# Performance work log

Measured on AMD Instinct MI355X. Metric: run time of the kernel, lower is better.

## Reference

```python
import jax, jax.numpy as jnp
import numpy as np

PS = 7  # patch (window) size
NH = 8  # num heads for local attention
EPS = 1e-5


def _rel_index(ps):
    # standard Swin-style relative position index over a ps x ps window
    coords = np.stack(np.meshgrid(np.arange(ps), np.arange(ps), indexing='ij'))  # (2,ps,ps)
    flat = coords.reshape(2, -1)                                # (2, ps*ps)
    rel = (flat[:, :, None] - flat[:, None, :]).transpose(1, 2, 0)  # (N,N,2)
    rel[..., 0] += ps - 1
    rel[..., 1] += ps - 1
    rel[..., 0] *= 2 * ps - 1
    return rel.sum(-1)  # (N,N) values in [0,(2ps-1)^2)

REL_IDX = jnp.asarray(_rel_index(PS))  # (49,49)


def _mha(x, qkv_w, qkv_b, proj_w, proj_b, num_heads, bias):
    # x: (Bn, N, C); weights stored (in,out)
    Bn, N, C = x.shape
    d = C // num_heads
    qkv = (x @ qkv_w + qkv_b).reshape(Bn, N, 3, num_heads, d).transpose(2, 0, 3, 1, 4)
    q, k, v = qkv[0], qkv[1], qkv[2]
    attn = jnp.einsum('bhnd,bhmd->bhnm', q, k) * (d ** -0.5)
    if bias is not None:
        attn = attn + bias
    attn = jax.nn.softmax(attn, axis=-1)
    out = jnp.einsum('bhnm,bhmd->bhnd', attn, v).transpose(0, 2, 1, 3).reshape(Bn, N, C)
    return out @ proj_w + proj_b


def setup_inputs() -> dict:
    key = jax.random.key(0)
    ks = jax.random.split(key, 8)
    B, C, H, W = 4, 256, 112, 112
    s = 0.02
    return {
        'x': jax.random.normal(ks[0], (B, C, H, W), jnp.float32),
        'norm_gamma': jnp.ones((C,), jnp.float32),
        'norm_beta': jnp.zeros((C,), jnp.float32),
        'qkv_l_w': jax.random.normal(ks[1], (C, 3 * C), jnp.float32) * s,
        'qkv_l_b': jnp.zeros((3 * C,), jnp.float32),
        'proj_l_w': jax.random.normal(ks[2], (C, C), jnp.float32) * s,
        'proj_l_b': jnp.zeros((C,), jnp.float32),
        'rpb_table': jax.random.normal(ks[3], ((2 * PS - 1) ** 2, NH), jnp.float32) * s,
        'qkv_c_w': jax.random.normal(ks[4], (PS * PS, 3 * PS * PS), jnp.float32) * s,
        'qkv_c_b': jnp.zeros((3 * PS * PS,), jnp.float32),
        'proj_c_w': jax.random.normal(ks[5], (PS * PS, PS * PS), jnp.float32) * s,
        'proj_c_b': jnp.zeros((PS * PS,), jnp.float32),
        'proj_w': jax.random.normal(ks[6], (2 * C, C), jnp.float32) * s,
    }


def reference(x, norm_gamma, norm_beta, qkv_l_w, qkv_l_b, proj_l_w, proj_l_b,
              rpb_table, qkv_c_w, qkv_c_b, proj_c_w, proj_c_b, proj_w):
    B, C, H, W = x.shape
    ps, N = PS, PS * PS
    nP = (H // ps) * (W // ps)
    shortcut = x

    # b c h w -> b h w c, then LayerNorm over C
    xt = x.transpose(0, 2, 3, 1)
    mu = xt.mean(-1, keepdims=True)
    var = xt.var(-1, keepdims=True)
    xn = (xt - mu) * jax.lax.rsqrt(var + EPS) * norm_gamma + norm_beta

    # window partition -> (B*nP, N, C)
    patches = xn.reshape(B, H // ps, ps, W // ps, ps, C)
    patches = patches.transpose(0, 1, 3, 2, 4, 5).reshape(-1, N, C)

    # local windowed attention with relative position bias
    bias = rpb_table[REL_IDX].transpose(2, 0, 1)[None]  # (1,NH,N,N)
    attn_local = _mha(patches, qkv_l_w, qkv_l_b, proj_l_w, proj_l_b, NH, bias)

    # cross-channel attention: (B*C, nP, N), dim=N, single head, no RPE
    pc = patches.reshape(B, nP, N, C).transpose(0, 3, 1, 2).reshape(B * C, nP, N)
    attn_cross = _mha(pc, qkv_c_w, qkv_c_b, proj_c_w, proj_c_b, 1, None)
    attn_cross = attn_cross.reshape(B, C, nP, N).transpose(0, 2, 3, 1).reshape(-1, N, C)

    def reverse(w):  # (B*nP, N, C) -> (B, H*W, C)
        w = w.reshape(B, H // ps, W // ps, ps, ps, C)
        return w.transpose(0, 1, 3, 2, 4, 5).reshape(B, H * W, C)

    out = jnp.concatenate([reverse(attn_local), reverse(attn_cross)], axis=-1) @ proj_w
    out = out.reshape(B, H, W, C).transpose(0, 3, 1, 2)
    return (out, shortcut)
```

## Files before the change

### kernel.cpp

```cpp
#include <hip/hip_runtime.h>
#include <hip/hip_bf16.h>


#define PS 7
#define NWIN_N 49
#define CH 256
#define HH 112
#define WW 112
#define BB 4
#define NHEAD 8
#define HD 32

static constexpr size_t ELEMS = (size_t)BB * CH * HH * WW;
static constexpr size_t SZ    = ELEMS * 2;

typedef __attribute__((ext_vector_type(8))) short short8;
typedef __attribute__((ext_vector_type(4))) float f32x4;

static __device__ __forceinline__ unsigned short bf16_bits(float v) {
    __hip_bfloat16 h = __float2bfloat16(v);
    return *reinterpret_cast<unsigned short*>(&h);
}

__global__ __launch_bounds__(256) void ln_partition_kernel(
    const float* __restrict__ x, const float* __restrict__ gamma,
    const float* __restrict__ beta, __hip_bfloat16* __restrict__ patches)
{
    int blk = blockIdx.x;
    int seg = blk % 7;
    int bh = blk / 7;
    int h = bh % HH, b = bh / HH;
    int w0 = seg * 16;
    int tid = threadIdx.x;

    __shared__ float X[256][17];
    __shared__ float mus[16], rstds[16];

    #pragma unroll
    for (int l = 0; l < 16; ++l) {
        int idx = l * 256 + tid;
        int c = idx >> 4, wl = idx & 15;
        X[c][wl] = x[((size_t)(b * CH + c) * HH + h) * WW + w0 + wl];
    }
    __syncthreads();

    if (tid < 16) {
        float s = 0.f, ss = 0.f;
        for (int c = 0; c < 256; ++c) { float v = X[c][tid]; s += v; ss += v * v; }
        float mu = s * (1.f / 256.f);
        float var = ss * (1.f / 256.f) - mu * mu;
        mus[tid] = mu;
        rstds[tid] = rsqrtf(var + 1e-5f);
    }
    __syncthreads();

    int c = tid;
    float g = gamma[c], be = beta[c];
    int hp = h / PS, r = h - hp * PS;
    #pragma unroll
    for (int wl = 0; wl < 16; ++wl) {
        int w = w0 + wl;
        int wp = w / PS, cc = w - wp * PS;
        int win = (b * 16 + hp) * 16 + wp;
        int i = r * PS + cc;
        float v = (X[c][wl] - mus[wl]) * rstds[wl] * g + be;
        patches[((size_t)win * NWIN_N + i) * CH + c] = __float2bfloat16(v);
    }
}

__global__ __launch_bounds__(256) void copy_f32_kernel(
    const float* __restrict__ x, float* __restrict__ out)
{
    size_t i = ((size_t)blockIdx.x * 256 + threadIdx.x) * 4;
    *(float4*)(out + i) = *(const float4*)(x + i);
}

__global__ __launch_bounds__(256) void prep_wt_kernel(
    const float* __restrict__ W, unsigned short* __restrict__ Wt,
    int Kreal, int N, int Kpad, int Npad)
{
    int idx = blockIdx.x * 256 + threadIdx.x;
    if (idx >= Npad * Kpad) return;
    int n = idx / Kpad, k = idx - n * Kpad;
    float v = (n < N && k < Kreal) ? W[(size_t)k * N + n] : 0.f;
    Wt[idx] = bf16_bits(v);
}

__global__ __launch_bounds__(256) void prep_wt_qkvc_kernel(
    const float* __restrict__ W, unsigned short* __restrict__ Wt)
{
    int idx = blockIdx.x * 256 + threadIdx.x;
    if (idx >= 192 * 64) return;
    int n = idx >> 6, k = idx & 63;
    int s = -1;
    if (n < 49) s = n;
    else if (n >= 56 && n < 105) s = n - 7;
    else if (n >= 112 && n < 161) s = n - 14;
    float v = (s >= 0 && k < 49) ? W[(size_t)k * 147 + s] : 0.f;
    Wt[idx] = bf16_bits(v);
}

__global__ __launch_bounds__(192) void prep_bias_c_kernel(
    const float* __restrict__ b, float* __restrict__ bc)
{
    int n = threadIdx.x;
    int s = -1;
    if (n < 49) s = n;
    else if (n >= 56 && n < 105) s = n - 7;
    else if (n >= 112 && n < 161) s = n - 14;
    bc[n] = (s >= 0) ? b[s] : 0.f;
}

__global__ __launch_bounds__(256) void bias_prep_kernel(
    const float* __restrict__ rpb, float* __restrict__ biasb)
{
    int idx = blockIdx.x * 256 + threadIdx.x;
    int head = idx >> 12;
    int rem = idx & 4095;
    int i = rem >> 6, j = rem & 63;
    float v;
    if (j >= NWIN_N) v = -1e9f;
    else if (i >= NWIN_N) v = 0.f;
    else {
        int ri = i / 7, ci = i - ri * 7;
        int rj = j / 7, cj = j - rj * 7;
        v = rpb[((ri - rj + 6) * 13 + (ci - cj + 6)) * NHEAD + head];
    }
    biasb[idx] = v;
}

__global__ __launch_bounds__(256) void pad49_kernel(
    const unsigned short* __restrict__ src, unsigned short* __restrict__ dst)
{
    size_t idx = (size_t)blockIdx.x * 256 + threadIdx.x;
    int t = idx & 63;
    size_t m = idx >> 6;
    dst[idx] = (t < 49) ? src[m * 49 + t] : (unsigned short)0;
}

__global__ __launch_bounds__(256) void gemm_mfma_kernel(
    const __hip_bfloat16* __restrict__ A1p, const __hip_bfloat16* __restrict__ A2p,
    int K1, const unsigned short* __restrict__ Wt, const float* __restrict__ bias,
    __hip_bfloat16* __restrict__ Cb, float* __restrict__ Cf,
    int M, int N, int K, int pitchN)
{
    __shared__ __align__(16) unsigned short Alds[128][72];
    __shared__ __align__(16) unsigned short Wlds[64][72];
    const unsigned short* A1 = (const unsigned short*)A1p;
    const unsigned short* A2 = (const unsigned short*)A2p;

    const int nb = gridDim.x;
    const int ntiles = nb * gridDim.y;
    const int bid = blockIdx.y * nb + blockIdx.x;
    const int chunk = ntiles >> 3;
    const int tile = (bid & 7) * chunk + (bid >> 3);
    const int m0 = (tile / nb) * 128, n0 = (tile % nb) * 64;

    const int tid = threadIdx.x, lane = tid & 63, wave = tid >> 6;
    const int wm = wave >> 1, wn = wave & 1;
    const int lr = lane & 15, lk = lane >> 4;

    f32x4 acc[4][2];
    #pragma unroll
    for (int i = 0; i < 4; ++i)
        #pragma unroll
        for (int j = 0; j < 2; ++j) acc[i][j] = (f32x4){0.f, 0.f, 0.f, 0.f};

    for (int k0 = 0; k0 < K; k0 += 64) {
        #pragma unroll
        for (int i = 0; i < 4; ++i) {
            int s = tid + 256 * i;
            int row = s >> 3, c8 = (s & 7) * 8;
            int k = k0 + c8;
            const unsigned short* src = (k < K1)
                ? A1 + (size_t)(m0 + row) * K1 + k
                : A2 + (size_t)(m0 + row) * (K - K1) + (k - K1);
            *(short8*)&Alds[row][c8] = *(const short8*)src;
        }
        #pragma unroll
        for (int i = 0; i < 2; ++i) {
            int s = tid + 256 * i;
            int row = s >> 3, c8 = (s & 7) * 8;
            *(short8*)&Wlds[row][c8] =
                *(const short8*)(Wt + (size_t)(n0 + row) * K + k0 + c8);
        }
        __syncthreads();
        #pragma unroll
        for (int kk = 0; kk < 64; kk += 32) {
            short8 a[4], w[2];
            #pragma unroll
            for (int mi = 0; mi < 4; ++mi)
                a[mi] = *(const short8*)&Alds[wm * 64 + mi * 16 + lr][kk + lk * 8];
            #pragma unroll
            for (int nj = 0; nj < 2; ++nj)
                w[nj] = *(const short8*)&Wlds[wn * 32 + nj * 16 + lr][kk + lk * 8];
            #pragma unroll
            for (int mi = 0; mi < 4; ++mi)
                #pragma unroll
                for (int nj = 0; nj < 2; ++nj)
                    acc[mi][nj] = __builtin_amdgcn_mfma_f32_16x16x32_bf16(
                        a[mi], w[nj], acc[mi][nj], 0, 0, 0);
        }
        __syncthreads();
    }

    if (Cb) {
        if ((pitchN & 7) == 0) {
            #pragma unroll
            for (int nj = 0; nj < 2; ++nj) {
                int n = n0 + wn * 32 + nj * 16 + lr;
                float bv = (bias && n < N) ? bias[n] : 0.f;
                #pragma unroll
                for (int mi = 0; mi < 4; ++mi)
                    #pragma unroll
                    for (int r = 0; r < 4; ++r)
                        Alds[wm * 64 + mi * 16 + lk * 4 + r][wn * 32 + nj * 16 + lr] =
                            bf16_bits(acc[mi][nj][r] + bv);
            }
            __syncthreads();
            #pragma unroll
            for (int i = 0; i < 4; ++i) {
                int s = tid + 256 * i;
                int row = s >> 3, c8 = (s & 7) * 8;
                if (n0 + c8 + 8 <= pitchN)
                    *(short8*)((unsigned short*)Cb + (size_t)(m0 + row) * pitchN + n0 + c8) =
                        *(const short8*)&Alds[row][c8];
            }
        } else {
            #pragma unroll
            for (int nj = 0; nj < 2; ++nj) {
                int n = n0 + wn * 32 + nj * 16 + lr;
                if (n >= N) continue;
                float bv = bias ? bias[n] : 0.f;
                #pragma unroll
                for (int mi = 0; mi < 4; ++mi) {
                    #pragma unroll
                    for (int r = 0; r < 4; ++r) {
                        int m = m0 + wm * 64 + mi * 16 + lk * 4 + r;
                        ((unsigned short*)Cb)[(size_t)m * pitchN + n] =
                            bf16_bits(acc[mi][nj][r] + bv);
                    }
                }
            }
        }
    } else {
        #pragma unroll
        for (int mi = 0; mi < 4; ++mi) {
            #pragma unroll
            for (int r = 0; r < 4; ++r) {
                int m = m0 + wm * 64 + mi * 16 + lk * 4 + r;
                int b = m / 12544, rem = m - b * 12544;
                int p = rem / 49, t = rem - p * 49;
                int h = (p >> 4) * 7 + t / 7, w = (p & 15) * 7 + (t % 7);
                size_t ob = ((size_t)(b * 256) * HH + h) * WW + w;
                #pragma unroll
                for (int nj = 0; nj < 2; ++nj) {
                    int ch = n0 + wn * 32 + nj * 16 + lr;
                    Cf[ob + (size_t)ch * (HH * WW)] = acc[mi][nj][r];
                }
            }
        }
    }
}

__global__ __launch_bounds__(64) void local_attn_mfma_kernel(
    const __hip_bfloat16* __restrict__ qkv,
    const float* __restrict__ biasb,
    __hip_bfloat16* __restrict__ outp)
{
    __shared__ __align__(16) unsigned short VT_lds[32][72];
    __shared__ __align__(16) unsigned short P_lds[16][72];

    const int win  = blockIdx.x >> 3;
    const int head = blockIdx.x & 7;
    const int lane = threadIdx.x;
    const int lr = lane & 15, lk = lane >> 4;
    const unsigned short* q16 = (const unsigned short*)qkv;
    const size_t rowbase = (size_t)win * NWIN_N;
    const float scale = 0.17677669529663687f;

    for (int t = 0; t < 32; ++t) {
        int idx = lane + 64 * t;
        int j = idx >> 5, d = idx & 31;
        unsigned short v = 0;
        if (j < NWIN_N) v = q16[(rowbase + j) * 768 + 512 + head * HD + d];
        VT_lds[d][j] = v;
    }

    short8 kf[4], qf[4];
    #pragma unroll
    for (int jt = 0; jt < 4; ++jt) {
        int j = jt * 16 + lr;
        short8 f = *(const short8*)(q16 + (rowbase + j) * 768 + 256 + head * HD + lk * 8);
        if (j >= NWIN_N) {
            #pragma unroll
            for (int e = 0; e < 8; ++e) f[e] = 0;
        }
        kf[jt] = f;
    }
    #pragma unroll
    for (int it = 0; it < 4; ++it) {
        int i = it * 16 + lr;
        qf[it] = *(const short8*)(q16 + (rowbase + i) * 768 + head * HD + lk * 8);
    }
    __syncthreads();

    #pragma unroll
    for (int it = 0; it < 4; ++it) {
        const int i = it * 16 + lr;
        f32x4 sacc[4];
        #pragma unroll
        for (int jt = 0; jt < 4; ++jt) {
            f32x4 z = (f32x4){0.f, 0.f, 0.f, 0.f};
            sacc[jt] = __builtin_amdgcn_mfma_f32_16x16x32_bf16(kf[jt], qf[it], z, 0, 0, 0);
        }
        const float* brow = biasb + head * 4096 + i * 64;
        float sv[4][4];
        float mt = -1e30f;
        #pragma unroll
        for (int jt = 0; jt < 4; ++jt) {
            float4 bv = *(const float4*)&brow[jt * 16 + lk * 4];
            sv[jt][0] = sacc[jt][0] * scale + bv.x;
            sv[jt][1] = sacc[jt][1] * scale + bv.y;
            sv[jt][2] = sacc[jt][2] * scale + bv.z;
            sv[jt][3] = sacc[jt][3] * scale + bv.w;
            #pragma unroll
            for (int r = 0; r < 4; ++r) mt = fmaxf(mt, sv[jt][r]);
        }
        mt = fmaxf(mt, __shfl_xor(mt, 16, 64));
        mt = fmaxf(mt, __shfl_xor(mt, 32, 64));
        float psum = 0.f;
        #pragma unroll
        for (int jt = 0; jt < 4; ++jt) {
            float p0 = __expf(sv[jt][0] - mt);
            float p1 = __expf(sv[jt][1] - mt);
            float p2 = __expf(sv[jt][2] - mt);
            float p3 = __expf(sv[jt][3] - mt);
            psum += (p0 + p1) + (p2 + p3);
            uint2 wv;
            wv.x = (unsigned)bf16_bits(p0) | ((unsigned)bf16_bits(p1) << 16);
            wv.y = (unsigned)bf16_bits(p2) | ((unsigned)bf16_bits(p3) << 16);
            *(uint2*)&P_lds[lr][jt * 16 + lk * 4] = wv;
        }
        psum += __shfl_xor(psum, 16, 64);
        psum += __shfl_xor(psum, 32, 64);
        __syncthreads();

        f32x4 oacc[2];
        oacc[0] = (f32x4){0.f, 0.f, 0.f, 0.f};
        oacc[1] = (f32x4){0.f, 0.f, 0.f, 0.f};
        #pragma unroll
        for (int kst = 0; kst < 2; ++kst) {
            short8 bfv = *(const short8*)&P_lds[lr][kst * 32 + lk * 8];
            #pragma unroll
            for (int dt = 0; dt < 2; ++dt) {
                short8 af = *(const short8*)&VT_lds[dt * 16 + lr][kst * 32 + lk * 8];
                oacc[dt] = __builtin_amdgcn_mfma_f32_16x16x32_bf16(af, bfv, oacc[dt], 0, 0, 0);
            }
        }
        if (i < NWIN_N) {
            float inv = 1.f / psum;
            unsigned short* orow = (unsigned short*)outp + (rowbase + i) * CH + head * HD;
            #pragma unroll
            for (int dt = 0; dt < 2; ++dt) {
                uint2 wv;
                wv.x = (unsigned)bf16_bits(oacc[dt][0] * inv)
                     | ((unsigned)bf16_bits(oacc[dt][1] * inv) << 16);
                wv.y = (unsigned)bf16_bits(oacc[dt][2] * inv)
                     | ((unsigned)bf16_bits(oacc[dt][3] * inv) << 16);
                *(uint2*)&orow[dt * 16 + lk * 4] = wv;
            }
        }
        __syncthreads();
    }
}

__global__ __launch_bounds__(256) void cross_attn_mfma_kernel(
    const __hip_bfloat16* __restrict__ qkv,
    __hip_bfloat16* __restrict__ outp)
{
    __shared__ __align__(16) unsigned short K_lds[64][72];
    __shared__ __align__(16) unsigned short VT_lds[64][72];
    __shared__ __align__(16) unsigned short P_lds[2][64][72];

    const int bc = blockIdx.x;
    const size_t base = (size_t)bc * 256;
    const int tid  = threadIdx.x;
    const int lane = tid & 63;
    const int wave = tid >> 6;
    const int i0w  = wave * 64;
    const int lr   = lane & 15;
    const int lk   = lane >> 4;
    const int prow = wave * 16 + lr;

    const unsigned short* q16 = (const unsigned short*)qkv;
    const float inv7 = 1.f / 7.f;
    const short8 zf = (short8){0, 0, 0, 0, 0, 0, 0, 0};

    short8 qf[4][2];
    #pragma unroll
    for (int it = 0; it < 4; ++it) {
        const unsigned short* qrow = q16 + (base + i0w + it * 16 + lr) * 168;
        #pragma unroll
        for (int kst = 0; kst < 2; ++kst) {
            int k0 = lk * 8 + kst * 32;
            qf[it][kst] = (k0 <= 48) ? *(const short8*)(qrow + k0) : zf;
        }
    }

    float m_run[4], l_run[4];
    f32x4 acc_o[4][4];
    #pragma unroll
    for (int it = 0; it < 4; ++it) { m_run[it] = -1e30f; l_run[it] = 0.f; }
    #pragma unroll
    for (int dt = 0; dt < 4; ++dt)
        #pragma unroll
        for (int it = 0; it < 4; ++it) acc_o[dt][it] = (f32x4){0.f, 0.f, 0.f, 0.f};

    for (int jt4 = 0; jt4 < 4; ++jt4) {
        const int j0 = jt4 * 64;
        {
            const int jr = tid >> 3, c8 = (tid & 7) * 8;
            #pragma unroll
            for (int h = 0; h < 2; ++h) {
                int jj = jr + h * 32;
                const unsigned short* row = q16 + (base + j0 + jj) * 168;
                *(short8*)&K_lds[jj][c8]    = (c8 <= 48) ? *(const short8*)(row + 56 + c8) : zf;
                *(short8*)&P_lds[0][jj][c8] = (c8 <= 48) ? *(const short8*)(row + 112 + c8) : zf;
            }
        }
        __syncthreads();
        {
            const int jj = tid & 63, dg = tid >> 6;
            #pragma unroll
            for (int e = 0; e < 16; ++e) {
                int d = dg * 16 + e;
                VT_lds[d][jj] = P_lds[0][jj][d];
            }
        }
        __syncthreads();

        #pragma unroll
        for (int it = 0; it < 4; ++it) {
            unsigned short* prowp = &P_lds[it & 1][prow][0];
            f32x4 sacc[4];
            #pragma unroll
            for (int jt = 0; jt < 4; ++jt) sacc[jt] = (f32x4){0.f, 0.f, 0.f, 0.f};
            #pragma unroll
            for (int kst = 0; kst < 2; ++kst) {
                #pragma unroll
                for (int jt = 0; jt < 4; ++jt) {
                    short8 af = *(const short8*)&K_lds[jt * 16 + lr][lk * 8 + kst * 32];
                    sacc[jt] = __builtin_amdgcn_mfma_f32_16x16x32_bf16(
                        af, qf[it][kst], sacc[jt], 0, 0, 0);
                }
            }
            float mt = -1e30f;
            #pragma unroll
            for (int jt = 0; jt < 4; ++jt)
                #pragma unroll
                for (int r = 0; r < 4; ++r) mt = fmaxf(mt, sacc[jt][r]);
            mt = fmaxf(mt, __shfl_xor(mt, 16, 64));
            mt = fmaxf(mt, __shfl_xor(mt, 32, 64));
            float mnew = fmaxf(m_run[it], mt * inv7);
            float corr = __expf(m_run[it] - mnew);
            m_run[it] = mnew;
            l_run[it] *= corr;
            #pragma unroll
            for (int dt = 0; dt < 4; ++dt)
                #pragma unroll
                for (int r = 0; r < 4; ++r) acc_o[dt][it][r] *= corr;

            float psum = 0.f;
            #pragma unroll
            for (int jt = 0; jt < 4; ++jt) {
                float p0 = __expf(sacc[jt][0] * inv7 - mnew);
                float p1 = __expf(sacc[jt][1] * inv7 - mnew);
                float p2 = __expf(sacc[jt][2] * inv7 - mnew);
                float p3 = __expf(sacc[jt][3] * inv7 - mnew);
                psum += (p0 + p1) + (p2 + p3);
                uint2 wv;
                wv.x = (unsigned)bf16_bits(p0) | ((unsigned)bf16_bits(p1) << 16);
                wv.y = (unsigned)bf16_bits(p2) | ((unsigned)bf16_bits(p3) << 16);
                *(uint2*)(prowp + jt * 16 + lk * 4) = wv;
            }
            psum += __shfl_xor(psum, 16, 64);
            psum += __shfl_xor(psum, 32, 64);
            l_run[it] += psum;

            #pragma unroll
            for (int kst = 0; kst < 2; ++kst) {
                short8 bfv = *(const short8*)(prowp + kst * 32 + lk * 8);
                #pragma unroll
                for (int dt = 0; dt < 4; ++dt) {
                    short8 af = *(const short8*)&VT_lds[dt * 16 + lr][kst * 32 + lk * 8];
                    acc_o[dt][it] = __builtin_amdgcn_mfma_f32_16x16x32_bf16(
                        af, bfv, acc_o[dt][it], 0, 0, 0);
                }
            }
        }
        __syncthreads();
    }

    #pragma unroll
    for (int it = 0; it < 4; ++it) {
        float inv = 1.f / l_run[it];
        unsigned short* orow = (unsigned short*)outp + (base + i0w + it * 16 + lr) * 64;
        #pragma unroll
        for (int dt = 0; dt < 4; ++dt) {
            uint2 wv;
            wv.x = (unsigned)bf16_bits(acc_o[dt][it][0] * inv)
                 | ((unsigned)bf16_bits(acc_o[dt][it][1] * inv) << 16);
            wv.y = (unsigned)bf16_bits(acc_o[dt][it][2] * inv)
                 | ((unsigned)bf16_bits(acc_o[dt][it][3] * inv) << 16);
            *(uint2*)&orow[dt * 16 + lk * 4] = wv;
        }
    }
}

__global__ __launch_bounds__(256) void transpose_bf16_kernel(
    const __hip_bfloat16* __restrict__ src, __hip_bfloat16* __restrict__ dst,
    int R, int Cc)
{
    __shared__ __hip_bfloat16 T[64][66];
    int b = blockIdx.z;
    int r0 = blockIdx.y * 64, c0 = blockIdx.x * 64;
    const __hip_bfloat16* s = src + (size_t)b * R * Cc;
    __hip_bfloat16* d = dst + (size_t)b * R * Cc;
    int tid = threadIdx.x;
    int lr = tid >> 6, lc = tid & 63;

    #pragma unroll
    for (int l = 0; l < 16; ++l) {
        int rr = l * 4 + lr;
        T[rr][lc] = s[(size_t)(r0 + rr) * Cc + c0 + lc];
    }
    __syncthreads();
    #pragma unroll
    for (int l = 0; l < 16; ++l) {
        int cc = l * 4 + lr;
        d[(size_t)(c0 + cc) * R + r0 + lc] = T[lc][cc];
    }
}

__global__ void ws_marker_kernel(float* __restrict__ out0)
{
    if (threadIdx.x == 0) out0[0] = 777.0f;
}

extern "C" void kernel_launch(void* const* d_in, const int* in_sizes, int n_in,
                              void* d_out, int out_size, void* d_ws, size_t ws_size,
                              hipStream_t stream)
{
    const float* x        = (const float*)d_in[0];
    const float* gamma    = (const float*)d_in[1];
    const float* beta     = (const float*)d_in[2];
    const float* qkv_l_w  = (const float*)d_in[3];
    const float* qkv_l_b  = (const float*)d_in[4];
    const float* proj_l_w = (const float*)d_in[5];
    const float* proj_l_b = (const float*)d_in[6];
    const float* rpb      = (const float*)d_in[7];
    const float* qkv_c_w  = (const float*)d_in[8];
    const float* qkv_c_b  = (const float*)d_in[9];
    const float* proj_c_w = (const float*)d_in[10];
    const float* proj_c_b = (const float*)d_in[11];
    const float* proj_w   = (const float*)d_in[12];

    float* out0 = (float*)d_out;
    float* out1 = out0 + ELEMS;

    copy_f32_kernel<<<(int)(ELEMS / 1024), 256, 0, stream>>>(x, out1);

    char* ws = (char*)d_ws;
    if (ws_size < 6 * SZ) {
        ws_marker_kernel<<<1, 64, 0, stream>>>(out0);
        return;
    }

    const size_t P = SZ;
    __hip_bfloat16* localOut  = (__hip_bfloat16*)(ws + 0 * P);
    unsigned short* wt_qkv_l  = (unsigned short*)(ws + 0 * P);
    float*          biasb     = (float*)(ws + 0 * P + 0x80000);
    __hip_bfloat16* patches   = (__hip_bfloat16*)(ws + 1 * P);
    __hip_bfloat16* qkv_l     = (__hip_bfloat16*)(ws + 2 * P);
    __hip_bfloat16* attnL     = (__hip_bfloat16*)(ws + 5 * P);
    char*           G         = ws + 4 * P + 0xB00000;
    unsigned short* wt_proj_l = (unsigned short*)(G + 0x000000);
    unsigned short* wt_qkv_c  = (unsigned short*)(G + 0x080000);
    unsigned short* wt_proj_c = (unsigned short*)(G + 0x100000);
    unsigned short* wt_final  = (unsigned short*)(G + 0x180000);
    float*          biasc     = (float*)(G + 0x300000);
    __hip_bfloat16* pc_dense  = (__hip_bfloat16*)(ws + 2 * P);
    __hip_bfloat16* pc_pad    = (__hip_bfloat16*)(ws + 6 * P - (size_t)262144 * 64 * 2);
    __hip_bfloat16* qkvc      = (__hip_bfloat16*)(ws + 1 * P);
    __hip_bfloat16* crossAttn = pc_pad;
    __hip_bfloat16* crossProj = (__hip_bfloat16*)(ws + 1 * P);
    __hip_bfloat16* crossT    = (__hip_bfloat16*)(ws + 2 * P);

    prep_wt_kernel<<<768, 256, 0, stream>>>(qkv_l_w, wt_qkv_l, 256, 768, 256, 768);
    bias_prep_kernel<<<128, 256, 0, stream>>>(rpb, biasb);
    ln_partition_kernel<<<BB * HH * 7, 256, 0, stream>>>(x, gamma, beta, patches);
    gemm_mfma_kernel<<<dim3(12, 392), 256, 0, stream>>>(
        patches, nullptr, 256, wt_qkv_l, qkv_l_b, qkv_l, nullptr, 50176, 768, 256, 768);
    local_attn_mfma_kernel<<<1024 * NHEAD, 64, 0, stream>>>(qkv_l, biasb, attnL);
    prep_wt_kernel<<<256, 256, 0, stream>>>(proj_l_w, wt_proj_l, 256, 256, 256, 256);
    prep_wt_qkvc_kernel<<<48, 256, 0, stream>>>(qkv_c_w, wt_qkv_c);
    prep_bias_c_kernel<<<1, 192, 0, stream>>>(qkv_c_b, biasc);
    prep_wt_kernel<<<16, 256, 0, stream>>>(proj_c_w, wt_proj_c, 49, 49, 64, 64);
    prep_wt_kernel<<<512, 256, 0, stream>>>(proj_w, wt_final, 512, 256, 512, 256);
    gemm_mfma_kernel<<<dim3(4, 392), 256, 0, stream>>>(
        attnL, nullptr, 256, wt_proj_l, proj_l_b, localOut, nullptr, 50176, 256, 256, 256);
    transpose_bf16_kernel<<<dim3(4, 196, BB), 256, 0, stream>>>(patches, pc_dense, 12544, 256);
    pad49_kernel<<<65536, 256, 0, stream>>>(
        (const unsigned short*)pc_dense, (unsigned short*)pc_pad);
    gemm_mfma_kernel<<<dim3(3, 2048), 256, 0, stream>>>(
        pc_pad, nullptr, 64, wt_qkv_c, biasc, qkvc, nullptr, 262144, 161, 64, 168);
    cross_attn_mfma_kernel<<<1024, 256, 0, stream>>>(qkvc, crossAttn);
    gemm_mfma_kernel<<<dim3(1, 2048), 256, 0, stream>>>(
        crossAttn, nullptr, 64, wt_proj_c, proj_c_b, crossProj, nullptr, 262144, 49, 64, 49);
    transpose_bf16_kernel<<<dim3(196, 4, BB), 256, 0, stream>>>(crossProj, crossT, 256, 12544);
    gemm_mfma_kernel<<<dim3(4, 392), 256, 0, stream>>>(
        localOut, crossT, 256, wt_final, nullptr, nullptr, out0, 50176, 256, 512, 256);
}
```

Baseline: 357.4 us.

## Use direct global-to-LDS loads with XOR swizzle in GEMM; fuse transpose and pad

The GEMM now stages A and W tiles with global_load_lds (direct global-to-LDS copies) into an unpadded, XOR-swizzled LDS layout, and the fragment reads and epilogue staging use the same swizzle. This drops the register round trip and the padded shared arrays. Separately, the transpose and the pad-to-64 step for the cross-channel path are merged into one kernel that writes the padded layout directly and zero-fills the tail columns, removing an intermediate buffer pass. Risks: global_load_lds places each lane's 16 bytes at consecutive LDS addresses, so the swizzle mapping must match exactly. The fused kernel also writes with a scattered 2-byte store pattern.

```diff
diff --git a/kernel.cpp b/kernel.cpp
--- a/kernel.cpp
+++ b/kernel.cpp
@@ -20,6 +20,12 @@
 static __device__ __forceinline__ unsigned short bf16_bits(float v) {
     __hip_bfloat16 h = __float2bfloat16(v);
     return *reinterpret_cast<unsigned short*>(&h);
+}
+
+static __device__ __forceinline__ void gload_lds16(const void* g, void* l) {
+    __builtin_amdgcn_global_load_lds(
+        (const __attribute__((address_space(1))) unsigned int*)g,
+        (__attribute__((address_space(3))) unsigned int*)l, 16, 0, 0);
 }
 
 __global__ __launch_bounds__(256) void ln_partition_kernel(
@@ -129,23 +135,14 @@
     biasb[idx] = v;
 }
 
-__global__ __launch_bounds__(256) void pad49_kernel(
-    const unsigned short* __restrict__ src, unsigned short* __restrict__ dst)
-{
-    size_t idx = (size_t)blockIdx.x * 256 + threadIdx.x;
-    int t = idx & 63;
-    size_t m = idx >> 6;
-    dst[idx] = (t < 49) ? src[m * 49 + t] : (unsigned short)0;
-}
-
 __global__ __launch_bounds__(256) void gemm_mfma_kernel(
     const __hip_bfloat16* __restrict__ A1p, const __hip_bfloat16* __restrict__ A2p,
     int K1, const unsigned short* __restrict__ Wt, const float* __restrict__ bias,
     __hip_bfloat16* __restrict__ Cb, float* __restrict__ Cf,
     int M, int N, int K, int pitchN)
 {
-    __shared__ __align__(16) unsigned short Alds[128][72];
-    __shared__ __align__(16) unsigned short Wlds[64][72];
+    __shared__ __align__(16) unsigned short Alds[128 * 64];
+    __shared__ __align__(16) unsigned short Wlds[64 * 64];
     const unsigned short* A1 = (const unsigned short*)A1p;
     const unsigned short* A2 = (const unsigned short*)A2p;
 
@@ -169,31 +166,39 @@
     for (int k0 = 0; k0 < K; k0 += 64) {
         #pragma unroll
         for (int i = 0; i < 4; ++i) {
-            int s = tid + 256 * i;
-            int row = s >> 3, c8 = (s & 7) * 8;
+            int s_lin = i * 256 + tid;
+            int row = s_lin >> 3, sl = s_lin & 7;
+            int c8 = ((sl ^ (row & 7)) << 3);
             int k = k0 + c8;
             const unsigned short* src = (k < K1)
                 ? A1 + (size_t)(m0 + row) * K1 + k
                 : A2 + (size_t)(m0 + row) * (K - K1) + (k - K1);
-            *(short8*)&Alds[row][c8] = *(const short8*)src;
+            gload_lds16(src, Alds + (size_t)(i * 256 + wave * 64) * 8);
         }
         #pragma unroll
         for (int i = 0; i < 2; ++i) {
-            int s = tid + 256 * i;
-            int row = s >> 3, c8 = (s & 7) * 8;
-            *(short8*)&Wlds[row][c8] =
-                *(const short8*)(Wt + (size_t)(n0 + row) * K + k0 + c8);
+            int s_lin = i * 256 + tid;
+            int row = s_lin >> 3, sl = s_lin & 7;
+            int c8 = ((sl ^ (row & 7)) << 3);
+            gload_lds16(Wt + (size_t)(n0 + row) * K + k0 + c8,
+                        Wlds + (size_t)(i * 256 + wave * 64) * 8);
         }
         __syncthreads();
         #pragma unroll
         for (int kk = 0; kk < 64; kk += 32) {
             short8 a[4], w[2];
             #pragma unroll
-            for (int mi = 0; mi < 4; ++mi)
-                a[mi] = *(const short8*)&Alds[wm * 64 + mi * 16 + lr][kk + lk * 8];
-            #pragma unroll
-            for (int nj = 0; nj < 2; ++nj)
-                w[nj] = *(const short8*)&Wlds[wn * 32 + nj * 16 + lr][kk + lk * 8];
+            for (int mi = 0; mi < 4; ++mi) {
+                int r = wm * 64 + mi * 16 + lr;
+                int sl = (kk >> 3) + lk;
+                a[mi] = *(const short8*)&Alds[(r << 6) + (((sl) ^ (r & 7)) << 3)];
+            }
+            #pragma unroll
+            for (int nj = 0; nj < 2; ++nj) {
+                int r = wn * 32 + nj * 16 + lr;
+                int sl = (kk >> 3) + lk;
+                w[nj] = *(const short8*)&Wlds[(r << 6) + (((sl) ^ (r & 7)) << 3)];
+            }
             #pragma unroll
             for (int mi = 0; mi < 4; ++mi)
                 #pragma unroll
@@ -210,21 +215,24 @@
             for (int nj = 0; nj < 2; ++nj) {
                 int n = n0 + wn * 32 + nj * 16 + lr;
                 float bv = (bias && n < N) ? bias[n] : 0.f;
+                int col = wn * 32 + nj * 16 + lr;
                 #pragma unroll
                 for (int mi = 0; mi < 4; ++mi)
                     #pragma unroll
-                    for (int r = 0; r < 4; ++r)
-                        Alds[wm * 64 + mi * 16 + lk * 4 + r][wn * 32 + nj * 16 + lr] =
-                            bf16_bits(acc[mi][nj][r] + bv);
+                    for (int r = 0; r < 4; ++r) {
+                        int row = wm * 64 + mi * 16 + lk * 4 + r;
+                        int idx = (row << 6) + (((col >> 3) ^ (row & 7)) << 3) + (col & 7);
+                        Alds[idx] = bf16_bits(acc[mi][nj][r] + bv);
+                    }
             }
             __syncthreads();
             #pragma unroll
             for (int i = 0; i < 4; ++i) {
                 int s = tid + 256 * i;
-                int row = s >> 3, c8 = (s & 7) * 8;
-                if (n0 + c8 + 8 <= pitchN)
-                    *(short8*)((unsigned short*)Cb + (size_t)(m0 + row) * pitchN + n0 + c8) =
-                        *(const short8*)&Alds[row][c8];
+                int row = s >> 3, sl = s & 7;
+                if (n0 + sl * 8 + 8 <= pitchN)
+                    *(short8*)((unsigned short*)Cb + (size_t)(m0 + row) * pitchN + n0 + sl * 8) =
+                        *(const short8*)&Alds[(row << 6) + (((sl) ^ (row & 7)) << 3)];
             }
         } else {
             #pragma unroll
@@ -514,6 +522,41 @@
             wv.y = (unsigned)bf16_bits(acc_o[dt][it][2] * inv)
                  | ((unsigned)bf16_bits(acc_o[dt][it][3] * inv) << 16);
             *(uint2*)&orow[dt * 16 + lk * 4] = wv;
+        }
+    }
+}
+
+__global__ __launch_bounds__(256) void transpose_pad_kernel(
+    const __hip_bfloat16* __restrict__ patches, unsigned short* __restrict__ pc_pad)
+{
+    __shared__ __hip_bfloat16 T[64][66];
+    int b = blockIdx.z;
+    int r0 = blockIdx.y * 64, c0 = blockIdx.x * 64;
+    const __hip_bfloat16* s = patches + (size_t)b * 12544 * 256;
+    int tid = threadIdx.x;
+    int lr4 = tid >> 6, lc = tid & 63;
+
+    #pragma unroll
+    for (int l = 0; l < 16; ++l) {
+        int rr = l * 4 + lr4;
+        T[rr][lc] = s[(size_t)(r0 + rr) * 256 + c0 + lc];
+    }
+    __syncthreads();
+    int r = r0 + lc;
+    int p = r / 49, t = r - p * 49;
+    #pragma unroll
+    for (int l = 0; l < 16; ++l) {
+        int cc = l * 4 + lr4;
+        size_t dst = (((size_t)(b * 256 + c0 + cc) * 256) + p) * 64 + t;
+        pc_pad[dst] = *(unsigned short*)&T[lc][cc];
+    }
+    int plo = r0 / 49, phi = (r0 + 63) / 49;
+    for (int pp = plo; pp <= phi; ++pp) {
+        if (pp >= 256) break;
+        for (int idx = tid; idx < 64 * 15; idx += 256) {
+            int cc = idx / 15, t2 = 49 + idx % 15;
+            size_t dst = (((size_t)(b * 256 + c0 + cc) * 256) + pp) * 64 + t2;
+            pc_pad[dst] = 0;
         }
     }
 }
@@ -590,7 +633,6 @@
     unsigned short* wt_proj_c = (unsigned short*)(G + 0x100000);
     unsigned short* wt_final  = (unsigned short*)(G + 0x180000);
     float*          biasc     = (float*)(G + 0x300000);
-    __hip_bfloat16* pc_dense  = (__hip_bfloat16*)(ws + 2 * P);
     __hip_bfloat16* pc_pad    = (__hip_bfloat16*)(ws + 6 * P - (size_t)262144 * 64 * 2);
     __hip_bfloat16* qkvc      = (__hip_bfloat16*)(ws + 1 * P);
     __hip_bfloat16* crossAttn = pc_pad;
@@ -610,9 +652,8 @@
     prep_wt_kernel<<<512, 256, 0, stream>>>(proj_w, wt_final, 512, 256, 512, 256);
     gemm_mfma_kernel<<<dim3(4, 392), 256, 0, stream>>>(
         attnL, nullptr, 256, wt_proj_l, proj_l_b, localOut, nullptr, 50176, 256, 256, 256);
-    transpose_bf16_kernel<<<dim3(4, 196, BB), 256, 0, stream>>>(patches, pc_dense, 12544, 256);
-    pad49_kernel<<<65536, 256, 0, stream>>>(
-        (const unsigned short*)pc_dense, (unsigned short*)pc_pad);
+    transpose_pad_kernel<<<dim3(4, 196, BB), 256, 0, stream>>>(
+        patches, (unsigned short*)pc_pad);
     gemm_mfma_kernel<<<dim3(3, 2048), 256, 0, stream>>>(
         pc_pad, nullptr, 64, wt_qkv_c, biasc, qkvc, nullptr, 262144, 161, 64, 168);
     cross_attn_mfma_kernel<<<1024, 256, 0, stream>>>(qkvc, crossAttn);
```

New measurement: 344.0 us. -3.8%, faster.
